# Kernel optimization log

Hardware: AMD Instinct MI355X
Metric: run time of the kernel (lower is better)

Reference implementation:

```python
import jax, jax.numpy as jnp
import numpy as np

N, F, A = 200000, 512, 8
DIM_L0 = A * (A + 1) // 2
ACTION_MIN, ACTION_MAX = -1.0, 1.0


def setup_inputs() -> dict:
    key = jax.random.key(0)
    ks = jax.random.split(key, 14)
    def rn(k, shape, scale=0.05):
        return (jax.random.normal(k, shape, dtype=jnp.float32) * scale)
    return {
        "X_in": jax.random.normal(ks[0], (N, F), dtype=jnp.float32),
        "RL_indice": (jax.random.uniform(ks[1], (N,)) < 0.5).astype(jnp.float32),
        "action": jax.random.normal(ks[2], (N,), dtype=jnp.float32),
        "W1": rn(ks[3], (F, 32)), "b1": rn(ks[4], (32,)),
        "W2": rn(ks[5], (32, 32)), "b2": rn(ks[6], (32,)),
        "Wv": rn(ks[7], (32, 1)), "bv": rn(ks[8], (1,)),
        "Wmu": rn(ks[9], (32, A)), "bmu": rn(ks[10], (A,)),
        "WL": rn(ks[11], (32, DIM_L0)), "bL": rn(ks[12], (DIM_L0,)),
    }


def reference(X_in, RL_indice, action, W1, b1, W2, b2, Wv, bv, Wmu, bmu, WL, bL):
    # 2-layer policy MLP with ReLU
    h = jax.nn.relu(X_in @ W1 + b1)          # [N,32]
    h = jax.nn.relu(h @ W2 + b2)             # [N,32]
    value = h @ Wv + bv                      # [N,1]
    mu = jnp.tanh(h @ Wmu + bmu)             # [N,A]
    L0 = jnp.tanh(h @ WL + bL)               # [N,DIM_L0]

    # scatter L0 into lower triangle, exponentiate the diagonal
    ti, tj = np.tril_indices(A)
    L = jnp.zeros((N, A, A), dtype=X_in.dtype).at[:, ti, tj].set(L0)
    d = np.arange(A)
    L = L.at[:, d, d].set(jnp.exp(L[:, d, d]))

    # NOTE: original code uses ELEMENTWISE product L * L^T (not matmul)
    P = L * jnp.swapaxes(L, 1, 2)            # [N,A,A]

    # quadratic-form advantage with provided action (broadcast scalar action)
    a = action[:, None] - mu                 # [N,A]
    Adv = -0.5 * jnp.einsum('na,nab,nb->n', a, P, a)[:, None]  # [N,1]
    Q = Adv + value                          # [N,1]

    # sample from MultivariateNormal(mu, inv(P)) via Cholesky reparam
    cov = jnp.linalg.inv(P)                  # [N,A,A]
    Lc = jnp.linalg.cholesky(cov)            # [N,A,A]
    z = jax.random.normal(jax.random.key(42), (N, A), dtype=X_in.dtype)
    samp = mu + jnp.einsum('nab,nb->na', Lc, z)
    samp = jnp.clip(samp, ACTION_MIN, ACTION_MAX)
    samp = samp * RL_indice[:, None]         # mask controlled vehicles
    return samp, Q, value
```

## Files before the change

### kernel.cpp

```cpp
#include <hip/hip_runtime.h>
#include <stdint.h>

#define TPB 256
#define FDIM 512
#define HD 32
#define AD 8
#define RPB 256
#define RT 32
#define NRT (RPB / RT)
#define H1P 40

typedef __bf16 bf16x8 __attribute__((ext_vector_type(8)));
typedef float f32x4 __attribute__((ext_vector_type(4)));
typedef uint32_t u32x4 __attribute__((ext_vector_type(4)));

#define BARRIER_LGKM() asm volatile("s_waitcnt lgkmcnt(0)\n\ts_barrier" ::: "memory")

__device__ __forceinline__ uint32_t rotl32(uint32_t x, int r) {
  return (x << r) | (x >> (32 - r));
}

__device__ __forceinline__ void tf2x32_key42(uint32_t& x0, uint32_t& x1) {
  const uint32_t ks0 = 0u, ks1 = 42u, ks2 = 0x1BD11BDAu ^ 0u ^ 42u;
  x0 += ks0; x1 += ks1;
#define TFR(r) { x0 += x1; x1 = rotl32(x1, (r)); x1 ^= x0; }
  TFR(13) TFR(15) TFR(26) TFR(6)
  x0 += ks1; x1 += ks2 + 1u;
  TFR(17) TFR(29) TFR(16) TFR(24)
  x0 += ks2; x1 += ks0 + 2u;
  TFR(13) TFR(15) TFR(26) TFR(6)
  x0 += ks0; x1 += ks1 + 3u;
  TFR(17) TFR(29) TFR(16) TFR(24)
  x0 += ks1; x1 += ks2 + 4u;
  TFR(13) TFR(15) TFR(26) TFR(6)
  x0 += ks2; x1 += ks0 + 5u;
#undef TFR
}

__device__ __forceinline__ float jax_normal_from_bits(uint32_t bits) {
  float u = __uint_as_float((bits >> 9) | 0x3f800000u) - 1.0f;
  const float lo = -0.99999994f;
  float v = fmaxf(lo, fmaf(u, 2.0f, lo));
  float w = -log1pf(-v * v);
  float p;
  if (w < 5.0f) {
    w -= 2.5f;
    p = 2.81022636e-08f;
    p = fmaf(p, w, 3.43273939e-07f);
    p = fmaf(p, w, -3.5233877e-06f);
    p = fmaf(p, w, -4.39150654e-06f);
    p = fmaf(p, w, 0.00021858087f);
    p = fmaf(p, w, -0.00125372503f);
    p = fmaf(p, w, -0.00417768164f);
    p = fmaf(p, w, 0.246640727f);
    p = fmaf(p, w, 1.50140941f);
  } else {
    w = sqrtf(w) - 3.0f;
    p = -0.000200214257f;
    p = fmaf(p, w, 0.000100950558f);
    p = fmaf(p, w, 0.00134934322f);
    p = fmaf(p, w, -0.00367342844f);
    p = fmaf(p, w, 0.00573950773f);
    p = fmaf(p, w, -0.0076224613f);
    p = fmaf(p, w, 0.00943887047f);
    p = fmaf(p, w, 1.00167406f);
    p = fmaf(p, w, 2.83297682f);
  }
  return 1.41421356f * (p * v);
}

__device__ __forceinline__ uint32_t bf2(float a, float b) {
  uint32_t ua = __float_as_uint(a);
  uint32_t ub = __float_as_uint(b);
  ua = (ua + 0x7fffu + ((ua >> 16) & 1u)) >> 16;
  ub = (ub + 0x7fffu + ((ub >> 16) & 1u)) >> 16;
  return ua | (ub << 16);
}

__device__ __forceinline__ uint16_t bf1(float x) {
  uint32_t u = __float_as_uint(x);
  return (uint16_t)((u + 0x7fffu + ((u >> 16) & 1u)) >> 16);
}

__device__ __forceinline__ bf16x8 pack8(float4 a, float4 b) {
  u32x4 r;
  r.x = bf2(a.x, a.y);
  r.y = bf2(a.z, a.w);
  r.z = bf2(b.x, b.y);
  r.w = bf2(b.z, b.w);
  return __builtin_bit_cast(bf16x8, r);
}

__global__ __launch_bounds__(TPB, 2) void naf_fused(
    const float* __restrict__ X, const float* __restrict__ RL,
    const float* __restrict__ act,
    const float* __restrict__ W1, const float* __restrict__ b1,
    const float* __restrict__ W2, const float* __restrict__ b2,
    const float* __restrict__ Wv, const float* __restrict__ bv,
    const float* __restrict__ Wmu, const float* __restrict__ bmu,
    const float* __restrict__ WL, const float* __restrict__ bL,
    float* __restrict__ out, int N) {
  __shared__ __align__(16) char sX[RT * 1024];
  __shared__ __align__(16) uint16_t sh1[RPB * H1P];
  __shared__ float sW2[HD * HD];
  __shared__ float sWmu[HD * AD];
  __shared__ float sWLd[HD * AD];
  __shared__ float sWv[HD];
  __shared__ float sb2[HD], sbmu[AD], sbLd[AD];
  __shared__ float sbv;

  const int tid  = threadIdx.x;
  const int lane = tid & 63;
  const int wid  = tid >> 6;
  const int llo  = lane & 15;
  const int lhi  = lane >> 4;
  const int m    = wid >> 1;
  const int nt   = wid & 1;
  const int R0   = blockIdx.x * RPB;

  const float4* Xv = reinterpret_cast<const float4*>(X);

#define LOADX(rg)                                                   \
  {                                                                 \
    _Pragma("unroll")                                               \
    for (int it = 0; it < 16; ++it) {                               \
      const int g = it * TPB + tid;        \
      const int rl = (rg) * RT + (g >> 7);                          \
      int r = R0 + rl;                                              \
      r = r < N ? r : (N - 1);                                      \
      xreg[it] = Xv[(size_t)r * (FDIM / 4) + (g & 127)];            \
    }                                                               \
  }

  float4 xreg[16];
  LOADX(0)

  bf16x8 bfrag[16];
  {
    const float* wcol = W1 + nt * 16 + llo;
#pragma unroll
    for (int kc = 0; kc < 16; ++kc) {
      const float* wp = wcol + (size_t)(kc * 32 + lhi * 8) * HD;
      float4 v0, v1;
      v0.x = wp[0 * HD]; v0.y = wp[1 * HD]; v0.z = wp[2 * HD]; v0.w = wp[3 * HD];
      v1.x = wp[4 * HD]; v1.y = wp[5 * HD]; v1.z = wp[6 * HD]; v1.w = wp[7 * HD];
      bfrag[kc] = pack8(v0, v1);
    }
  }
  const float b1c = b1[nt * 16 + llo];

  for (int i = tid; i < HD * HD; i += TPB) sW2[i] = W2[i];
  if (tid < 256) {
    sWmu[tid] = Wmu[tid];
    const int k = tid >> 3, a = tid & 7;
    sWLd[tid] = WL[k * 36 + ((a * a + 3 * a) >> 1)];
  }
  if (tid < HD) { sWv[tid] = Wv[tid]; sb2[tid] = b2[tid]; }
  if (tid < AD) { sbmu[tid] = bmu[tid]; sbLd[tid] = bL[(tid * tid + 3 * tid) >> 1]; }
  if (tid == 0) sbv = bv[0];

#pragma unroll 1
  for (int rg = 0; rg < NRT; ++rg) {
#pragma unroll
    for (int it = 0; it < 16; ++it) {
      const int g = it * TPB + tid;
      const int row = g >> 7;
      const int col4 = g & 127;
      uint2 pkd = make_uint2(bf2(xreg[it].x, xreg[it].y),
                             bf2(xreg[it].z, xreg[it].w));
      const int boff = (col4 * 8) ^ ((row & 7) << 4);
      *reinterpret_cast<uint2*>(sX + row * 1024 + boff) = pkd;
    }
    if (rg + 1 < NRT) LOADX(rg + 1)
    BARRIER_LGKM();

    f32x4 acc = (f32x4){0.0f, 0.0f, 0.0f, 0.0f};
    const int arow = m * 16 + llo;
    const char* abase = sX + arow * 1024;
    const int aswz = (llo & 7) << 4;
#pragma unroll
    for (int kc = 0; kc < 16; ++kc) {
      bf16x8 afrag = *reinterpret_cast<const bf16x8*>(
          abase + ((kc * 64 + lhi * 16) ^ aswz));
      acc = __builtin_amdgcn_mfma_f32_16x16x32_bf16(afrag, bfrag[kc], acc, 0, 0, 0);
    }

#pragma unroll
    for (int i = 0; i < 4; ++i) {
      const int rowl = rg * RT + m * 16 + lhi * 4 + i;
      sh1[rowl * H1P + nt * 16 + llo] = bf1(fmaxf(acc[i] + b1c, 0.0f));
    }
    BARRIER_LGKM();
  }

  const int row = R0 + tid;
  if (row >= N) return;

  float h1v[HD];
  {
    const uint16_t* hp = &sh1[tid * H1P];
#pragma unroll
    for (int q = 0; q < 4; ++q) {
      u32x4 u = *reinterpret_cast<const u32x4*>(hp + q * 8);
#pragma unroll
      for (int j = 0; j < 4; ++j) {
        const uint32_t wv = u[j];
        h1v[q * 8 + 2 * j]     = __uint_as_float(wv << 16);
        h1v[q * 8 + 2 * j + 1] = __uint_as_float(wv & 0xffff0000u);
      }
    }
  }

  float acc2[HD];
#pragma unroll
  for (int c = 0; c < HD; ++c) acc2[c] = 0.0f;
  {
    const float4* w2v = reinterpret_cast<const float4*>(sW2);
#pragma unroll 4
    for (int k = 0; k < HD; ++k) {
      const float hk = h1v[k];
#pragma unroll
      for (int q = 0; q < HD / 4; ++q) {
        float4 wv = w2v[k * (HD / 4) + q];
        acc2[4 * q + 0] = fmaf(hk, wv.x, acc2[4 * q + 0]);
        acc2[4 * q + 1] = fmaf(hk, wv.y, acc2[4 * q + 1]);
        acc2[4 * q + 2] = fmaf(hk, wv.z, acc2[4 * q + 2]);
        acc2[4 * q + 3] = fmaf(hk, wv.w, acc2[4 * q + 3]);
      }
    }
  }
  float h2[HD];
#pragma unroll
  for (int c = 0; c < HD; ++c) h2[c] = fmaxf(acc2[c] + sb2[c], 0.0f);

  float vacc = 0.0f;
  float mua[AD], dva[AD];
#pragma unroll
  for (int a = 0; a < AD; ++a) { mua[a] = 0.0f; dva[a] = 0.0f; }
  {
    const float4* wmu4 = reinterpret_cast<const float4*>(sWmu);
    const float4* wld4 = reinterpret_cast<const float4*>(sWLd);
#pragma unroll 4
    for (int k = 0; k < HD; ++k) {
      const float hk = h2[k];
      vacc = fmaf(hk, sWv[k], vacc);
      float4 m0 = wmu4[2 * k], m1 = wmu4[2 * k + 1];
      float4 l0 = wld4[2 * k], l1 = wld4[2 * k + 1];
      mua[0] = fmaf(hk, m0.x, mua[0]); mua[1] = fmaf(hk, m0.y, mua[1]);
      mua[2] = fmaf(hk, m0.z, mua[2]); mua[3] = fmaf(hk, m0.w, mua[3]);
      mua[4] = fmaf(hk, m1.x, mua[4]); mua[5] = fmaf(hk, m1.y, mua[5]);
      mua[6] = fmaf(hk, m1.z, mua[6]); mua[7] = fmaf(hk, m1.w, mua[7]);
      dva[0] = fmaf(hk, l0.x, dva[0]); dva[1] = fmaf(hk, l0.y, dva[1]);
      dva[2] = fmaf(hk, l0.z, dva[2]); dva[3] = fmaf(hk, l0.w, dva[3]);
      dva[4] = fmaf(hk, l1.x, dva[4]); dva[5] = fmaf(hk, l1.y, dva[5]);
      dva[6] = fmaf(hk, l1.z, dva[6]); dva[7] = fmaf(hk, l1.w, dva[7]);
    }
  }
  vacc += sbv;

  const float actn = act[row];
  const float rl_mask = RL[row];
  float adv = 0.0f;
  float smp[AD];
#pragma unroll
  for (int a = 0; a < AD; ++a) {
    const float mu = tanhf(mua[a] + sbmu[a]);
    const float dd = tanhf(dva[a] + sbLd[a]);
    const float ld = expf(dd);
    const float am = actn - mu;
    adv = fmaf(am * am, ld * ld, adv);
    const uint32_t e = (uint32_t)row * AD + (uint32_t)a;
    uint32_t x0 = 0u;
    uint32_t x1 = e;
    tf2x32_key42(x0, x1);
    const float z = jax_normal_from_bits(x0 ^ x1);
    float s = fmaf(z, 1.0f / ld, mu);
    s = fminf(fmaxf(s, -1.0f), 1.0f) * rl_mask;
    smp[a] = s;
  }
  const float q = fmaf(-0.5f, adv, vacc);

  float4* so = reinterpret_cast<float4*>(out) + (size_t)row * 2;
  so[0] = make_float4(smp[0], smp[1], smp[2], smp[3]);
  so[1] = make_float4(smp[4], smp[5], smp[6], smp[7]);
  out[(size_t)N * AD + row] = q;
  out[(size_t)N * AD + (size_t)N + row] = vacc;
#undef LOADX
}

extern "C" void kernel_launch(void* const* d_in, const int* in_sizes, int n_in,
                              void* d_out, int out_size, void* d_ws, size_t ws_size,
                              hipStream_t stream) {
  const float* X   = (const float*)d_in[0];
  const float* RL  = (const float*)d_in[1];
  const float* act = (const float*)d_in[2];
  const float* W1  = (const float*)d_in[3];
  const float* b1  = (const float*)d_in[4];
  const float* W2  = (const float*)d_in[5];
  const float* b2  = (const float*)d_in[6];
  const float* Wv  = (const float*)d_in[7];
  const float* bv  = (const float*)d_in[8];
  const float* Wmu = (const float*)d_in[9];
  const float* bmu = (const float*)d_in[10];
  const float* WL  = (const float*)d_in[11];
  const float* bL  = (const float*)d_in[12];
  const int N = in_sizes[1];
  const int blocks = (N + RPB - 1) / RPB;
  hipLaunchKernelGGL(naf_fused, dim3(blocks), dim3(TPB), 0, stream,
                     X, RL, act, W1, b1, W2, b2, Wv, bv, Wmu, bmu, WL, bL,
                     (float*)d_out, N);
}
```

Before: 112.7 us.

## Split X prefetch into two half-tile buffers, read small weights from global, raise occupancy

The X staging loop now uses two 8-register prefetch buffers, one per 16-row half of each 32-row tile. Each half is written to LDS and then its next load is issued, so global loads are interleaved more finely with LDS writes. The small layer-2 and head weights are no longer staged in shared memory and are read directly from global memory through uniform loads, which removes the LDS footprint and the setup stores. Launch bounds go from 2 to 3 blocks per CU to allow more waves in flight. The cost is fewer registers per thread and scalar/global weight loads in the per-row tail.

```diff
diff --git a/kernel.cpp b/kernel.cpp
--- a/kernel.cpp
+++ b/kernel.cpp
@@ -6,8 +6,6 @@
 #define HD 32
 #define AD 8
 #define RPB 256
-#define RT 32
-#define NRT (RPB / RT)
 #define H1P 40
 
 typedef __bf16 bf16x8 __attribute__((ext_vector_type(8)));
@@ -91,7 +89,7 @@
   return __builtin_bit_cast(bf16x8, r);
 }
 
-__global__ __launch_bounds__(TPB, 2) void naf_fused(
+__global__ __launch_bounds__(TPB, 3) void naf_fused(
     const float* __restrict__ X, const float* __restrict__ RL,
     const float* __restrict__ act,
     const float* __restrict__ W1, const float* __restrict__ b1,
@@ -100,14 +98,8 @@
     const float* __restrict__ Wmu, const float* __restrict__ bmu,
     const float* __restrict__ WL, const float* __restrict__ bL,
     float* __restrict__ out, int N) {
-  __shared__ __align__(16) char sX[RT * 1024];
+  __shared__ __align__(16) char sX[32 * 1024];
   __shared__ __align__(16) uint16_t sh1[RPB * H1P];
-  __shared__ float sW2[HD * HD];
-  __shared__ float sWmu[HD * AD];
-  __shared__ float sWLd[HD * AD];
-  __shared__ float sWv[HD];
-  __shared__ float sb2[HD], sbmu[AD], sbLd[AD];
-  __shared__ float sbv;
 
   const int tid  = threadIdx.x;
   const int lane = tid & 63;
@@ -120,20 +112,34 @@
 
   const float4* Xv = reinterpret_cast<const float4*>(X);
 
-#define LOADX(rg)                                                   \
+#define LOADX(xr, g)                                                \
   {                                                                 \
     _Pragma("unroll")                                               \
-    for (int it = 0; it < 16; ++it) {                               \
-      const int g = it * TPB + tid;        \
-      const int rl = (rg) * RT + (g >> 7);                          \
-      int r = R0 + rl;                                              \
+    for (int it = 0; it < 8; ++it) {                                \
+      const int idx = it * TPB + tid;                               \
+      int r = R0 + (g) * 16 + (idx >> 7);                           \
       r = r < N ? r : (N - 1);                                      \
-      xreg[it] = Xv[(size_t)r * (FDIM / 4) + (g & 127)];            \
+      xr[it] = Xv[(size_t)r * (FDIM / 4) + (idx & 127)];            \
     }                                                               \
   }
 
-  float4 xreg[16];
-  LOADX(0)
+#define WRITEX(xr, g)                                               \
+  {                                                                 \
+    _Pragma("unroll")                                               \
+    for (int it = 0; it < 8; ++it) {                                \
+      const int idx = it * TPB + tid;                               \
+      const int rig = idx >> 7;                \
+      const int col4 = idx & 127;                                   \
+      uint2 pkd = make_uint2(bf2(xr[it].x, xr[it].y),               \
+                             bf2(xr[it].z, xr[it].w));              \
+      const int boff = (col4 * 8) ^ ((rig & 7) << 4);               \
+      *reinterpret_cast<uint2*>(sX + (((g) & 1) * 16 + rig) * 1024 + boff) = pkd; \
+    }                                                               \
+  }
+
+  float4 xA[8], xB[8];
+  LOADX(xA, 0)
+  LOADX(xB, 1)
 
   bf16x8 bfrag[16];
   {
@@ -149,29 +155,12 @@
   }
   const float b1c = b1[nt * 16 + llo];
 
-  for (int i = tid; i < HD * HD; i += TPB) sW2[i] = W2[i];
-  if (tid < 256) {
-    sWmu[tid] = Wmu[tid];
-    const int k = tid >> 3, a = tid & 7;
-    sWLd[tid] = WL[k * 36 + ((a * a + 3 * a) >> 1)];
-  }
-  if (tid < HD) { sWv[tid] = Wv[tid]; sb2[tid] = b2[tid]; }
-  if (tid < AD) { sbmu[tid] = bmu[tid]; sbLd[tid] = bL[(tid * tid + 3 * tid) >> 1]; }
-  if (tid == 0) sbv = bv[0];
-
 #pragma unroll 1
-  for (int rg = 0; rg < NRT; ++rg) {
-#pragma unroll
-    for (int it = 0; it < 16; ++it) {
-      const int g = it * TPB + tid;
-      const int row = g >> 7;
-      const int col4 = g & 127;
-      uint2 pkd = make_uint2(bf2(xreg[it].x, xreg[it].y),
-                             bf2(xreg[it].z, xreg[it].w));
-      const int boff = (col4 * 8) ^ ((row & 7) << 4);
-      *reinterpret_cast<uint2*>(sX + row * 1024 + boff) = pkd;
-    }
-    if (rg + 1 < NRT) LOADX(rg + 1)
+  for (int t = 0; t < 8; ++t) {
+    WRITEX(xA, 2 * t)
+    if (t < 7) LOADX(xA, 2 * t + 2)
+    WRITEX(xB, 2 * t + 1)
+    if (t < 7) LOADX(xB, 2 * t + 3)
     BARRIER_LGKM();
 
     f32x4 acc = (f32x4){0.0f, 0.0f, 0.0f, 0.0f};
@@ -187,7 +176,7 @@
 
 #pragma unroll
     for (int i = 0; i < 4; ++i) {
-      const int rowl = rg * RT + m * 16 + lhi * 4 + i;
+      const int rowl = t * 32 + m * 16 + lhi * 4 + i;
       sh1[rowl * H1P + nt * 16 + llo] = bf1(fmaxf(acc[i] + b1c, 0.0f));
     }
     BARRIER_LGKM();
@@ -215,7 +204,7 @@
 #pragma unroll
   for (int c = 0; c < HD; ++c) acc2[c] = 0.0f;
   {
-    const float4* w2v = reinterpret_cast<const float4*>(sW2);
+    const float4* w2v = reinterpret_cast<const float4*>(W2);
 #pragma unroll 4
     for (int k = 0; k < HD; ++k) {
       const float hk = h1v[k];
@@ -231,32 +220,29 @@
   }
   float h2[HD];
 #pragma unroll
-  for (int c = 0; c < HD; ++c) h2[c] = fmaxf(acc2[c] + sb2[c], 0.0f);
+  for (int c = 0; c < HD; ++c) h2[c] = fmaxf(acc2[c] + b2[c], 0.0f);
 
   float vacc = 0.0f;
   float mua[AD], dva[AD];
 #pragma unroll
   for (int a = 0; a < AD; ++a) { mua[a] = 0.0f; dva[a] = 0.0f; }
   {
-    const float4* wmu4 = reinterpret_cast<const float4*>(sWmu);
-    const float4* wld4 = reinterpret_cast<const float4*>(sWLd);
+    const float4* wmu4 = reinterpret_cast<const float4*>(Wmu);
 #pragma unroll 4
     for (int k = 0; k < HD; ++k) {
       const float hk = h2[k];
-      vacc = fmaf(hk, sWv[k], vacc);
+      vacc = fmaf(hk, Wv[k], vacc);
       float4 m0 = wmu4[2 * k], m1 = wmu4[2 * k + 1];
-      float4 l0 = wld4[2 * k], l1 = wld4[2 * k + 1];
       mua[0] = fmaf(hk, m0.x, mua[0]); mua[1] = fmaf(hk, m0.y, mua[1]);
       mua[2] = fmaf(hk, m0.z, mua[2]); mua[3] = fmaf(hk, m0.w, mua[3]);
       mua[4] = fmaf(hk, m1.x, mua[4]); mua[5] = fmaf(hk, m1.y, mua[5]);
       mua[6] = fmaf(hk, m1.z, mua[6]); mua[7] = fmaf(hk, m1.w, mua[7]);
-      dva[0] = fmaf(hk, l0.x, dva[0]); dva[1] = fmaf(hk, l0.y, dva[1]);
-      dva[2] = fmaf(hk, l0.z, dva[2]); dva[3] = fmaf(hk, l0.w, dva[3]);
-      dva[4] = fmaf(hk, l1.x, dva[4]); dva[5] = fmaf(hk, l1.y, dva[5]);
-      dva[6] = fmaf(hk, l1.z, dva[6]); dva[7] = fmaf(hk, l1.w, dva[7]);
-    }
-  }
-  vacc += sbv;
+#pragma unroll
+      for (int a = 0; a < AD; ++a)
+        dva[a] = fmaf(hk, WL[k * 36 + ((a * a + 3 * a) >> 1)], dva[a]);
+    }
+  }
+  vacc += bv[0];
 
   const float actn = act[row];
   const float rl_mask = RL[row];
@@ -264,8 +250,8 @@
   float smp[AD];
 #pragma unroll
   for (int a = 0; a < AD; ++a) {
-    const float mu = tanhf(mua[a] + sbmu[a]);
-    const float dd = tanhf(dva[a] + sbLd[a]);
+    const float mu = tanhf(mua[a] + bmu[a]);
+    const float dd = tanhf(dva[a] + bL[(a * a + 3 * a) >> 1]);
     const float ld = expf(dd);
     const float am = actn - mu;
     adv = fmaf(am * am, ld * ld, adv);
@@ -286,6 +272,7 @@
   out[(size_t)N * AD + row] = q;
   out[(size_t)N * AD + (size_t)N + row] = vacc;
 #undef LOADX
+#undef WRITEX
 }
 
 extern "C" void kernel_launch(void* const* d_in, const int* in_sizes, int n_in,
```

Result: slower. 150.0 us (+33.1%).
